# Kernel tuning notes

Measured on AMD Instinct MI355X. Metric: run time of the kernel, lower is better.

Reference implementation:

```python
import jax, jax.numpy as jnp
import numpy as np

EMBED_DIM = 64  # scale factor dim (matches head dim)


def setup_inputs() -> dict:
    key0 = jax.random.key(0)
    kq, kk, kv = jax.random.split(key0, 3)
    shape = (2, 16, 2048, 64)  # [B, H, S, D]
    return {
        "query": jax.random.normal(kq, shape, dtype=jnp.float32),
        "key": jax.random.normal(kk, shape, dtype=jnp.float32),
        "value": jax.random.normal(kv, shape, dtype=jnp.float32),
    }


def reference(query, key, value):
    # qk = Q K^T / sqrt(embed_dim); softmax over last dim; @ V
    inv_scale = jnp.sqrt(jnp.asarray(EMBED_DIM, dtype=query.dtype))
    scores = jnp.einsum("bhqd,bhkd->bhqk", query, key) / inv_scale
    probs = jax.nn.softmax(scores, axis=-1)
    # dropout_p=0.0 -> identity (eval semantics)
    return jnp.einsum("bhqk,bhkd->bhqd", probs, value)
```

## Files before the change

### kernel.cpp

```cpp
#include <hip/hip_runtime.h>
#include <hip/hip_bf16.h>

#define S_LEN 2048
#define DDIM  64
#define SCALE 0.125f

typedef __attribute__((ext_vector_type(8))) short short8;
typedef __attribute__((ext_vector_type(4))) short short4v;
typedef __attribute__((ext_vector_type(4))) float floatx4;

__device__ __forceinline__ short f2bf(float f) {
    union { float f; unsigned u; } v; v.f = f;
    return (short)((v.u + 0x7fffu + ((v.u >> 16) & 1u)) >> 16);
}

__device__ __forceinline__ void dma16(const void* g, void* l) {
    __builtin_amdgcn_global_load_lds(
        (const __attribute__((address_space(1))) void*)g,
        (__attribute__((address_space(3))) void*)l, 16, 0, 0);
}

__global__ __launch_bounds__(256) void convert_k(const float* __restrict__ in,
                                                 short* __restrict__ out) {
    const size_t i = ((size_t)blockIdx.x * 256 + threadIdx.x) * 8;
    float4 a = *(const float4*)(in + i);
    float4 b = *(const float4*)(in + i + 4);
    short8 o;
    o[0]=f2bf(a.x); o[1]=f2bf(a.y); o[2]=f2bf(a.z); o[3]=f2bf(a.w);
    o[4]=f2bf(b.x); o[5]=f2bf(b.y); o[6]=f2bf(b.z); o[7]=f2bf(b.w);
    *(short8*)(out + i) = o;
}

__global__ __launch_bounds__(256) void transpose_v(const float* __restrict__ V,
                                                   short* __restrict__ Vt) {
    __shared__ short T[64 * 68];
    const int bh = blockIdx.x & 31;
    const int st = blockIdx.x >> 5;
    const int t  = threadIdx.x;
    const float* src = V + (size_t)bh * (S_LEN * DDIM) + (size_t)st * 64 * DDIM;

    const int skey = t >> 2, scol = (t & 3) * 4;
    #pragma unroll
    for (int i = 0; i < 4; ++i) {
        const int c = scol + i * 16;
        float4 v = *(const float4*)(src + (size_t)skey * 64 + c);
        short4v o; o[0]=f2bf(v.x); o[1]=f2bf(v.y); o[2]=f2bf(v.z); o[3]=f2bf(v.w);
        *(short4v*)&T[skey * 68 + c] = o;
    }
    __syncthreads();

    const int d = t >> 2, cb = (t & 3) * 16;
    short8 o0, o1;
    #pragma unroll
    for (int j = 0; j < 8; ++j) {
        o0[j] = T[(cb + j) * 68 + d];
        o1[j] = T[(cb + 8 + j) * 68 + d];
    }
    short* dst = Vt + (size_t)bh * (DDIM * S_LEN) + (size_t)d * S_LEN + st * 64 + cb;
    *(short8*)dst       = o0;
    *(short8*)(dst + 8) = o1;
}

__global__ __launch_bounds__(256) void attn_fast(
    const float* __restrict__ Q, const short* __restrict__ Kb,
    const short* __restrict__ Vt, float* __restrict__ O)
{
    __shared__ short Ks[2][64 * 64];
    __shared__ short Vs[2][64 * 64];
    __shared__ short Pl[4][32 * 72];

    const int tid  = threadIdx.x;
    const int wave = tid >> 6;
    const int lane = tid & 63;
    const int l16  = lane & 15;
    const int quad = lane >> 4;
    const int x7   = l16 & 7;

    const int bh = blockIdx.x & 31;
    const int qt = blockIdx.x >> 5;
    const size_t base = (size_t)bh * (S_LEN * DDIM);

    const int ci0 = tid,        r0 = ci0 >> 3, c0 = (ci0 & 7) ^ (r0 & 7);
    const int ci1 = 256 + tid,  r1 = ci1 >> 3, c1 = (ci1 & 7) ^ (r1 & 7);
    const short* pK0 = Kb + base + r0 * 64 + c0 * 8;
    const short* pK1 = Kb + base + r1 * 64 + c1 * 8;
    const short* pV0 = Vt + base + (size_t)r0 * S_LEN + c0 * 8;
    const short* pV1 = Vt + base + (size_t)r1 * S_LEN + c1 * 8;

    dma16(pK0, &Ks[0][ci0 * 8]);
    dma16(pK1, &Ks[0][ci1 * 8]);
    dma16(pV0, &Vs[0][ci0 * 8]);
    dma16(pV1, &Vs[0][ci1 * 8]);

    short8 qf[2][2];
    #pragma unroll
    for (int mt = 0; mt < 2; ++mt) {
        const float* qp = Q + base + (size_t)(qt * 128 + wave * 32 + mt * 16 + l16) * 64 + quad * 8;
        #pragma unroll
        for (int kt = 0; kt < 2; ++kt) {
            float4 a = *(const float4*)(qp + kt * 32);
            float4 b = *(const float4*)(qp + kt * 32 + 4);
            short* d = (short*)&qf[mt][kt];
            d[0]=f2bf(a.x*SCALE); d[1]=f2bf(a.y*SCALE); d[2]=f2bf(a.z*SCALE); d[3]=f2bf(a.w*SCALE);
            d[4]=f2bf(b.x*SCALE); d[5]=f2bf(b.y*SCALE); d[6]=f2bf(b.z*SCALE); d[7]=f2bf(b.w*SCALE);
        }
    }

    floatx4 oacc[2][4];
    float rs[2][4];
    #pragma unroll
    for (int mt = 0; mt < 2; ++mt) {
        #pragma unroll
        for (int dt = 0; dt < 4; ++dt) oacc[mt][dt] = (floatx4){0.f,0.f,0.f,0.f};
        #pragma unroll
        for (int r = 0; r < 4; ++r) rs[mt][r] = 0.f;
    }

    for (int kb = 0; kb < S_LEN / 64; ++kb) {
        const int cur = kb & 1;
        __syncthreads();

        if (kb + 1 < S_LEN / 64) {
            const int nxt = cur ^ 1;
            const int ok = (kb + 1) * (64 * 64), ov = (kb + 1) * 64;
            dma16(pK0 + ok, &Ks[nxt][ci0 * 8]);
            dma16(pK1 + ok, &Ks[nxt][ci1 * 8]);
            dma16(pV0 + ov, &Vs[nxt][ci0 * 8]);
            dma16(pV1 + ov, &Vs[nxt][ci1 * 8]);
        }

        const short* ks = Ks[cur];
        floatx4 sc[2][4];
        #pragma unroll
        for (int nt = 0; nt < 4; ++nt) {
            floatx4 a0 = (floatx4){0.f,0.f,0.f,0.f};
            floatx4 a1 = (floatx4){0.f,0.f,0.f,0.f};
            #pragma unroll
            for (int kt = 0; kt < 2; ++kt) {
                const int csw = (kt * 4 + quad) ^ x7;
                short8 kf = *(const short8*)&ks[(nt * 16 + l16) * 64 + csw * 8];
                a0 = __builtin_amdgcn_mfma_f32_16x16x32_bf16(qf[0][kt], kf, a0, 0, 0, 0);
                a1 = __builtin_amdgcn_mfma_f32_16x16x32_bf16(qf[1][kt], kf, a1, 0, 0, 0);
            }
            sc[0][nt] = a0; sc[1][nt] = a1;
        }

        short* Pw = &Pl[wave][0];
        #pragma unroll
        for (int mt = 0; mt < 2; ++mt) {
            #pragma unroll
            for (int r = 0; r < 4; ++r) {
                const int prow = (mt * 16 + quad * 4 + r) * 72;
                #pragma unroll
                for (int nt = 0; nt < 4; ++nt) {
                    float p = __expf(sc[mt][nt][r]);
                    rs[mt][r] += p;
                    Pw[prow + nt * 16 + l16] = f2bf(p);
                }
            }
        }

        const short* vs = Vs[cur];
        #pragma unroll
        for (int kt = 0; kt < 2; ++kt) {
            short8 pf0 = *(const short8*)&Pw[(l16)      * 72 + kt * 32 + quad * 8];
            short8 pf1 = *(const short8*)&Pw[(16 + l16) * 72 + kt * 32 + quad * 8];
            const int csw = (kt * 4 + quad) ^ x7;
            #pragma unroll
            for (int dt = 0; dt < 4; ++dt) {
                short8 vf = *(const short8*)&vs[(dt * 16 + l16) * 64 + csw * 8];
                oacc[0][dt] = __builtin_amdgcn_mfma_f32_16x16x32_bf16(pf0, vf, oacc[0][dt], 0, 0, 0);
                oacc[1][dt] = __builtin_amdgcn_mfma_f32_16x16x32_bf16(pf1, vf, oacc[1][dt], 0, 0, 0);
            }
        }
    }

    #pragma unroll
    for (int mt = 0; mt < 2; ++mt) {
        #pragma unroll
        for (int r = 0; r < 4; ++r) {
            float s = rs[mt][r];
            s += __shfl_xor(s, 1, 64);
            s += __shfl_xor(s, 2, 64);
            s += __shfl_xor(s, 4, 64);
            s += __shfl_xor(s, 8, 64);
            const float inv = 1.0f / s;
            const int row = qt * 128 + wave * 32 + mt * 16 + quad * 4 + r;
            float* op = O + base + (size_t)row * 64 + l16;
            #pragma unroll
            for (int dt = 0; dt < 4; ++dt)
                op[dt * 16] = oacc[mt][dt][r] * inv;
        }
    }
}

#define BQ    64
#define BKEY  64
#define KPAD  72

__global__ __launch_bounds__(256) void attn_kernel(
    const float* __restrict__ Q, const float* __restrict__ K,
    const float* __restrict__ V, float* __restrict__ O)
{
    __shared__ short Ksh[BKEY * KPAD];
    __shared__ short Vtt[DDIM * KPAD];
    __shared__ short Pls[4][16 * KPAD];

    const int tid  = threadIdx.x;
    const int wave = tid >> 6;
    const int lane = tid & 63;
    const int l16  = lane & 15;
    const int quad = lane >> 4;

    const int bh = blockIdx.x & 31;
    const int qt = blockIdx.x >> 5;
    const size_t base = (size_t)bh * S_LEN * DDIM;

    const int qrow = qt * BQ + wave * 16 + l16;
    short8 qf[2];
    {
        const float* qp = Q + base + (size_t)qrow * DDIM + quad * 8;
        #pragma unroll
        for (int kt = 0; kt < 2; ++kt) {
            float4 a = *(const float4*)(qp + kt * 32);
            float4 b = *(const float4*)(qp + kt * 32 + 4);
            short* d = (short*)&qf[kt];
            d[0]=f2bf(a.x*SCALE); d[1]=f2bf(a.y*SCALE); d[2]=f2bf(a.z*SCALE); d[3]=f2bf(a.w*SCALE);
            d[4]=f2bf(b.x*SCALE); d[5]=f2bf(b.y*SCALE); d[6]=f2bf(b.z*SCALE); d[7]=f2bf(b.w*SCALE);
        }
    }

    float m_i[4], l_i[4];
    floatx4 oacc[4];
    #pragma unroll
    for (int r = 0; r < 4; ++r) { m_i[r] = -3.0e38f; l_i[r] = 0.f; }
    #pragma unroll
    for (int dt = 0; dt < 4; ++dt) oacc[dt] = (floatx4){0.f, 0.f, 0.f, 0.f};

    const int skey = tid >> 2;
    const int scol = (tid & 3) * 4;

    for (int kb = 0; kb < S_LEN / BKEY; ++kb) {
        const float* Kg = K + base + (size_t)kb * BKEY * DDIM + (size_t)skey * DDIM;
        const float* Vg = V + base + (size_t)kb * BKEY * DDIM + (size_t)skey * DDIM;
        #pragma unroll
        for (int i = 0; i < 4; ++i) {
            const int c = scol + i * 16;
            float4 kv = *(const float4*)(Kg + c);
            short* kd = &Ksh[skey * KPAD + c];
            kd[0]=f2bf(kv.x); kd[1]=f2bf(kv.y); kd[2]=f2bf(kv.z); kd[3]=f2bf(kv.w);
            float4 vv = *(const float4*)(Vg + c);
            Vtt[(c+0)*KPAD + skey] = f2bf(vv.x);
            Vtt[(c+1)*KPAD + skey] = f2bf(vv.y);
            Vtt[(c+2)*KPAD + skey] = f2bf(vv.z);
            Vtt[(c+3)*KPAD + skey] = f2bf(vv.w);
        }
        __syncthreads();

        floatx4 sc[4];
        #pragma unroll
        for (int nt = 0; nt < 4; ++nt) {
            floatx4 acc = (floatx4){0.f, 0.f, 0.f, 0.f};
            #pragma unroll
            for (int kt = 0; kt < 2; ++kt) {
                short8 kf = *(const short8*)&Ksh[(nt*16 + l16) * KPAD + kt*32 + quad*8];
                acc = __builtin_amdgcn_mfma_f32_16x16x32_bf16(qf[kt], kf, acc, 0, 0, 0);
            }
            sc[nt] = acc;
        }

        short* Pw = &Pls[wave][0];
        #pragma unroll
        for (int r = 0; r < 4; ++r) {
            float mx = fmaxf(fmaxf(sc[0][r], sc[1][r]), fmaxf(sc[2][r], sc[3][r]));
            #pragma unroll
            for (int off = 1; off < 16; off <<= 1)
                mx = fmaxf(mx, __shfl_xor(mx, off, 64));
            const float mnew  = fmaxf(m_i[r], mx);
            const float alpha = __expf(m_i[r] - mnew);
            m_i[r] = mnew;
            float rsum = 0.f;
            #pragma unroll
            for (int nt = 0; nt < 4; ++nt) {
                float p = __expf(sc[nt][r] - mnew);
                rsum += p;
                Pw[(quad*4 + r) * KPAD + nt*16 + l16] = f2bf(p);
            }
            #pragma unroll
            for (int off = 1; off < 16; off <<= 1)
                rsum += __shfl_xor(rsum, off, 64);
            l_i[r] = l_i[r] * alpha + rsum;
            oacc[0][r] *= alpha; oacc[1][r] *= alpha;
            oacc[2][r] *= alpha; oacc[3][r] *= alpha;
        }

        #pragma unroll
        for (int kt = 0; kt < 2; ++kt) {
            short8 pf = *(const short8*)&Pw[l16 * KPAD + kt*32 + quad*8];
            #pragma unroll
            for (int dt = 0; dt < 4; ++dt) {
                short8 vf = *(const short8*)&Vtt[(dt*16 + l16) * KPAD + kt*32 + quad*8];
                oacc[dt] = __builtin_amdgcn_mfma_f32_16x16x32_bf16(pf, vf, oacc[dt], 0, 0, 0);
            }
        }
        __syncthreads();
    }

    #pragma unroll
    for (int r = 0; r < 4; ++r) {
        const float inv = 1.0f / l_i[r];
        const int row = qt * BQ + wave * 16 + quad * 4 + r;
        float* op = O + base + (size_t)row * DDIM + l16;
        #pragma unroll
        for (int dt = 0; dt < 4; ++dt)
            op[dt * 16] = oacc[dt][r] * inv;
    }
}

extern "C" void kernel_launch(void* const* d_in, const int* in_sizes, int n_in,
                              void* d_out, int out_size, void* d_ws, size_t ws_size,
                              hipStream_t stream) {
    const float* Q = (const float*)d_in[0];
    const float* K = (const float*)d_in[1];
    const float* V = (const float*)d_in[2];
    float* O = (float*)d_out;

    const size_t n_elem = (size_t)32 * S_LEN * DDIM;
    const size_t need = n_elem * 2 * 2;

    if (ws_size >= need) {
        short* Kb = (short*)d_ws;
        short* Vtp = (short*)d_ws + n_elem;
        convert_k<<<dim3((unsigned)(n_elem / (256 * 8))), dim3(256), 0, stream>>>(K, Kb);
        transpose_v<<<dim3(1024), dim3(256), 0, stream>>>(V, Vtp);
        attn_fast<<<dim3(512), dim3(256), 0, stream>>>(Q, Kb, Vtp, O);
    } else {
        attn_kernel<<<dim3(1024), dim3(256), 0, stream>>>(Q, K, V, O);
    }
}
```

Measured before the change: 154.8 us.

## Software-pipeline PV matmul one block behind QK, fuse K/V prep, use exp2

Restructures the attention main loop so the P·V MFMA for the previous key block runs after the current block's QK^T, with V loaded one stage later than K. This lets exp work overlap with matrix work and hides LDS latency. Folds log2(e) into the Q scale so the kernel can call the hardware exp2 directly. Merges the K conversion and V transpose into a single prep kernel, saving one launch. The price is an extra epilogue PV step plus a barrier, and the order of buffer reuse gets more delicate.

Result: slower. 157.9 us (+2.0%).

```diff
diff --git a/kernel.cpp b/kernel.cpp
--- a/kernel.cpp
+++ b/kernel.cpp
@@ -3,7 +3,9 @@
 
 #define S_LEN 2048
 #define DDIM  64
-#define SCALE 0.125f
+#define NT    (S_LEN / 64)
+#define SCALE  0.125f
+#define SCALE2 0.18033688f
 
 typedef __attribute__((ext_vector_type(8))) short short8;
 typedef __attribute__((ext_vector_type(4))) short short4v;
@@ -12,6 +14,14 @@
 __device__ __forceinline__ short f2bf(float f) {
     union { float f; unsigned u; } v; v.f = f;
     return (short)((v.u + 0x7fffu + ((v.u >> 16) & 1u)) >> 16);
+}
+
+__device__ __forceinline__ float fexp2(float x) {
+#if __has_builtin(__builtin_amdgcn_exp2f)
+    return __builtin_amdgcn_exp2f(x);
+#else
+    return exp2f(x);
+#endif
 }
 
 __device__ __forceinline__ void dma16(const void* g, void* l) {
@@ -20,25 +30,31 @@
         (__attribute__((address_space(3))) void*)l, 16, 0, 0);
 }
 
-__global__ __launch_bounds__(256) void convert_k(const float* __restrict__ in,
-                                                 short* __restrict__ out) {
-    const size_t i = ((size_t)blockIdx.x * 256 + threadIdx.x) * 8;
-    float4 a = *(const float4*)(in + i);
-    float4 b = *(const float4*)(in + i + 4);
-    short8 o;
-    o[0]=f2bf(a.x); o[1]=f2bf(a.y); o[2]=f2bf(a.z); o[3]=f2bf(a.w);
-    o[4]=f2bf(b.x); o[5]=f2bf(b.y); o[6]=f2bf(b.z); o[7]=f2bf(b.w);
-    *(short8*)(out + i) = o;
-}
-
-__global__ __launch_bounds__(256) void transpose_v(const float* __restrict__ V,
-                                                   short* __restrict__ Vt) {
+__global__ __launch_bounds__(256) void prep_kv(const float* __restrict__ K,
+                                               const float* __restrict__ V,
+                                               short* __restrict__ Kb,
+                                               short* __restrict__ Vt) {
     __shared__ short T[64 * 68];
     const int bh = blockIdx.x & 31;
     const int st = blockIdx.x >> 5;
     const int t  = threadIdx.x;
-    const float* src = V + (size_t)bh * (S_LEN * DDIM) + (size_t)st * 64 * DDIM;
-
+    const size_t tile_off = (size_t)bh * (S_LEN * DDIM) + (size_t)st * (64 * DDIM);
+
+    {
+        const float* src = K + tile_off + t * 16;
+        short* dst = Kb + tile_off + t * 16;
+        #pragma unroll
+        for (int h = 0; h < 2; ++h) {
+            float4 a = *(const float4*)(src + h * 8);
+            float4 b = *(const float4*)(src + h * 8 + 4);
+            short8 o;
+            o[0]=f2bf(a.x); o[1]=f2bf(a.y); o[2]=f2bf(a.z); o[3]=f2bf(a.w);
+            o[4]=f2bf(b.x); o[5]=f2bf(b.y); o[6]=f2bf(b.z); o[7]=f2bf(b.w);
+            *(short8*)(dst + h * 8) = o;
+        }
+    }
+
+    const float* src = V + tile_off;
     const int skey = t >> 2, scol = (t & 3) * 4;
     #pragma unroll
     for (int i = 0; i < 4; ++i) {
@@ -48,7 +64,6 @@
         *(short4v*)&T[skey * 68 + c] = o;
     }
     __syncthreads();
-
     const int d = t >> 2, cb = (t & 3) * 16;
     short8 o0, o1;
     #pragma unroll
@@ -89,8 +104,6 @@
 
     dma16(pK0, &Ks[0][ci0 * 8]);
     dma16(pK1, &Ks[0][ci1 * 8]);
-    dma16(pV0, &Vs[0][ci0 * 8]);
-    dma16(pV1, &Vs[0][ci1 * 8]);
 
     short8 qf[2][2];
     #pragma unroll
@@ -101,8 +114,8 @@
             float4 a = *(const float4*)(qp + kt * 32);
             float4 b = *(const float4*)(qp + kt * 32 + 4);
             short* d = (short*)&qf[mt][kt];
-            d[0]=f2bf(a.x*SCALE); d[1]=f2bf(a.y*SCALE); d[2]=f2bf(a.z*SCALE); d[3]=f2bf(a.w*SCALE);
-            d[4]=f2bf(b.x*SCALE); d[5]=f2bf(b.y*SCALE); d[6]=f2bf(b.z*SCALE); d[7]=f2bf(b.w*SCALE);
+            d[0]=f2bf(a.x*SCALE2); d[1]=f2bf(a.y*SCALE2); d[2]=f2bf(a.z*SCALE2); d[3]=f2bf(a.w*SCALE2);
+            d[4]=f2bf(b.x*SCALE2); d[5]=f2bf(b.y*SCALE2); d[6]=f2bf(b.z*SCALE2); d[7]=f2bf(b.w*SCALE2);
         }
     }
 
@@ -116,17 +129,21 @@
         for (int r = 0; r < 4; ++r) rs[mt][r] = 0.f;
     }
 
-    for (int kb = 0; kb < S_LEN / 64; ++kb) {
+    short* Pw = &Pl[wave][0];
+
+    for (int kb = 0; kb < NT; ++kb) {
         const int cur = kb & 1;
         __syncthreads();
 
-        if (kb + 1 < S_LEN / 64) {
-            const int nxt = cur ^ 1;
-            const int ok = (kb + 1) * (64 * 64), ov = (kb + 1) * 64;
-            dma16(pK0 + ok, &Ks[nxt][ci0 * 8]);
-            dma16(pK1 + ok, &Ks[nxt][ci1 * 8]);
-            dma16(pV0 + ov, &Vs[nxt][ci0 * 8]);
-            dma16(pV1 + ov, &Vs[nxt][ci1 * 8]);
+        if (kb + 1 < NT) {
+            const int ok = (kb + 1) * (64 * 64);
+            dma16(pK0 + ok, &Ks[cur ^ 1][ci0 * 8]);
+            dma16(pK1 + ok, &Ks[cur ^ 1][ci1 * 8]);
+        }
+        {
+            const int ov = kb * 64;
+            dma16(pV0 + ov, &Vs[cur][ci0 * 8]);
+            dma16(pV1 + ov, &Vs[cur][ci1 * 8]);
         }
 
         const short* ks = Ks[cur];
@@ -145,22 +162,47 @@
             sc[0][nt] = a0; sc[1][nt] = a1;
         }
 
-        short* Pw = &Pl[wave][0];
-        #pragma unroll
-        for (int mt = 0; mt < 2; ++mt) {
+        if (kb > 0) {
+            const short* vs = Vs[cur ^ 1];
+            #pragma unroll
+            for (int kt = 0; kt < 2; ++kt) {
+                short8 pf0 = *(const short8*)&Pw[(l16)      * 72 + kt * 32 + quad * 8];
+                short8 pf1 = *(const short8*)&Pw[(16 + l16) * 72 + kt * 32 + quad * 8];
+                const int csw = (kt * 4 + quad) ^ x7;
+                #pragma unroll
+                for (int dt = 0; dt < 4; ++dt) {
+                    short8 vf = *(const short8*)&vs[(dt * 16 + l16) * 64 + csw * 8];
+                    oacc[0][dt] = __builtin_amdgcn_mfma_f32_16x16x32_bf16(pf0, vf, oacc[0][dt], 0, 0, 0);
+                    oacc[1][dt] = __builtin_amdgcn_mfma_f32_16x16x32_bf16(pf1, vf, oacc[1][dt], 0, 0, 0);
+                }
+            }
+        }
+
+        short preg[2][4][4];
+        #pragma unroll
+        for (int mt = 0; mt < 2; ++mt)
+            #pragma unroll
+            for (int r = 0; r < 4; ++r)
+                #pragma unroll
+                for (int nt = 0; nt < 4; ++nt) {
+                    float p = fexp2(sc[mt][nt][r]);
+                    rs[mt][r] += p;
+                    preg[mt][r][nt] = f2bf(p);
+                }
+        #pragma unroll
+        for (int mt = 0; mt < 2; ++mt)
             #pragma unroll
             for (int r = 0; r < 4; ++r) {
                 const int prow = (mt * 16 + quad * 4 + r) * 72;
                 #pragma unroll
-                for (int nt = 0; nt < 4; ++nt) {
-                    float p = __expf(sc[mt][nt][r]);
-                    rs[mt][r] += p;
-                    Pw[prow + nt * 16 + l16] = f2bf(p);
-                }
-            }
-        }
-
-        const short* vs = Vs[cur];
+                for (int nt = 0; nt < 4; ++nt)
+                    Pw[prow + nt * 16 + l16] = preg[mt][r][nt];
+            }
+    }
+
+    __syncthreads();
+    {
+        const short* vs = Vs[(NT - 1) & 1];
         #pragma unroll
         for (int kt = 0; kt < 2; ++kt) {
             short8 pf0 = *(const short8*)&Pw[(l16)      * 72 + kt * 32 + quad * 8];
@@ -331,8 +373,7 @@
     if (ws_size >= need) {
         short* Kb = (short*)d_ws;
         short* Vtp = (short*)d_ws + n_elem;
-        convert_k<<<dim3((unsigned)(n_elem / (256 * 8))), dim3(256), 0, stream>>>(K, Kb);
-        transpose_v<<<dim3(1024), dim3(256), 0, stream>>>(V, Vtp);
+        prep_kv<<<dim3(1024), dim3(256), 0, stream>>>(K, V, Kb, Vtp);
         attn_fast<<<dim3(512), dim3(256), 0, stream>>>(Q, Kb, Vtp, O);
     } else {
         attn_kernel<<<dim3(1024), dim3(256), 0, stream>>>(Q, K, V, O);
```
